# Optimization experiments

Hardware: AMD Instinct MI355X
Metric: run time of the kernel (lower is better)

## Reference

```python
import jax, jax.numpy as jnp
import numpy as np

N = 20480      # total nodes
E = 327680     # total edges (avg degree 16)
B = 16         # graphs in batch
IN = 16        # node feature dim
H = 8          # hidden_out_channel
CO = 64        # conv_out_channel
ET = 36        # n_edge_types
EF = 2         # edge_features
OUT = 1        # classifier out
DIMS = [(IN, H), (H, H), (H, H), (H, CO)]


def setup_inputs() -> dict:
    key = jax.random.key(0)
    ks = jax.random.split(key, 32)
    inp = {}
    inp['x'] = jax.random.normal(ks[0], (N, IN), jnp.float32)
    inp['edge_index'] = jax.random.randint(ks[1], (2, E), 0, N)
    inp['edge_type'] = jax.random.randint(ks[2], (E,), 0, ET)
    inp['edge_attr'] = jax.random.normal(ks[3], (E, EF), jnp.float32)
    inp['cell_type'] = jax.random.randint(ks[4], (N,), 0, 2)
    inp['batch'] = (jnp.arange(N) // (N // B)).astype(jnp.int32)
    i = 5
    for l, (ci, co) in enumerate(DIMS, 1):
        d = ci * co
        s = 1.0 / np.sqrt(EF)
        inp[f'emb{l}'] = jax.random.normal(ks[i], (ET, d), jnp.float32) * 0.02; i += 1
        inp[f'wh{l}'] = jax.random.normal(ks[i], (EF, d), jnp.float32) * s; i += 1
        inp[f'bh{l}'] = jnp.zeros((d,), jnp.float32)
        inp[f'wg{l}'] = jax.random.normal(ks[i], (EF, d), jnp.float32) * s; i += 1
        inp[f'bg{l}'] = jnp.zeros((d,), jnp.float32)
        inp[f'root{l}'] = jax.random.normal(ks[i], (ci, co), jnp.float32) / np.sqrt(ci); i += 1
        inp[f'bias{l}'] = jnp.zeros((co,), jnp.float32)
    inp['clf_w'] = jax.random.normal(ks[i], (CO, OUT), jnp.float32) / np.sqrt(CO)
    inp['clf_b'] = jnp.zeros((OUT,), jnp.float32)
    return inp


def edge_weights(etype, ef, emb, wh, bh, wg, bg):
    # EdgeNN: relu(embedding(type) * fc_h(feat) + fc_g(feat)) -> [E, cin*cout]
    return jax.nn.relu(emb[etype] * (ef @ wh + bh) + (ef @ wg + bg))


def nnconv(h, src, dst, W, root, bias):
    # NNConv(aggr='mean', root_weight=True): gather src feats, per-edge matmul, scatter-mean
    cin, cout = root.shape
    msg = jnp.einsum('ei,eio->eo', h[src], W.reshape(-1, cin, cout))  # [E, cout]
    agg = jax.ops.segment_sum(msg, dst, num_segments=N)
    deg = jax.ops.segment_sum(jnp.ones_like(msg[:, 0]), dst, num_segments=N)
    return agg / jnp.maximum(deg, 1.0)[:, None] + h @ root + bias


def reference(x, edge_index, edge_type, edge_attr, cell_type, batch,
              emb1, wh1, bh1, wg1, bg1, root1, bias1,
              emb2, wh2, bh2, wg2, bg2, root2, bias2,
              emb3, wh3, bh3, wg3, bg3, root3, bias3,
              emb4, wh4, bh4, wg4, bg4, root4, bias4,
              clf_w, clf_b):
    src, dst = edge_index[0], edge_index[1]
    layers = [(emb1, wh1, bh1, wg1, bg1, root1, bias1),
              (emb2, wh2, bh2, wg2, bg2, root2, bias2),
              (emb3, wh3, bh3, wg3, bg3, root3, bias3),
              (emb4, wh4, bh4, wg4, bg4, root4, bias4)]
    h = x
    for (emb, wh, bh, wg, bg, root, bias) in layers:  # fixed 4 structurally-distinct layers
        W = edge_weights(edge_type, edge_attr, emb, wh, bh, wg, bg)
        h = jax.nn.relu(nnconv(h, src, dst, W, root, bias))
    # gated scatter-mean pooling over tumor cells (cell_type == 1)
    gate = (cell_type == 1).astype(jnp.int32)
    seg = gate * (batch.astype(jnp.int32) + 1)  # 0 = masked-out bucket
    pooled = jax.ops.segment_sum(h, seg, num_segments=B + 1)
    cnt = jax.ops.segment_sum(jnp.ones((h.shape[0],), h.dtype), seg, num_segments=B + 1)
    pooled = (pooled / jnp.maximum(cnt, 1.0)[:, None])[1:B + 1]  # [B, CO]
    return jax.nn.sigmoid(pooled @ clf_w + clf_b)  # hazards [B, OUT]
```

## Files before the change

### kernel.cpp

```cpp
#include <hip/hip_runtime.h>
#include <math.h>

#define NN 20480
#define NE 327680
#define NBATCH 16

typedef float v2f __attribute__((ext_vector_type(2)));

static __device__ __forceinline__ v2f vmax0(v2f a) {
  v2f r; r.x = fmaxf(a.x, 0.f); r.y = fmaxf(a.y, 0.f); return r;
}
#define VMAX0 vmax0

__global__ __launch_bounds__(256) void prep_kernel(
    const int* __restrict__ dst, int* __restrict__ cnt,
    const float* __restrict__ e4, float* __restrict__ t4) {
  int b = blockIdx.x;
  if (b < NE / 256) {
    int e = b * 256 + threadIdx.x;
    atomicAdd(&cnt[dst[e]], 1);
  } else {
    int idx = (b - NE / 256) * 256 + threadIdx.x;
    int t = idx >> 9, r = idx & 511, o = r >> 3, i = r & 7;
    t4[idx] = e4[(t << 9) + i * 64 + o];
  }
}

__global__ __launch_bounds__(1024) void scan_kernel(const int* __restrict__ cnt,
                                                    int* __restrict__ off,
                                                    int* __restrict__ cur,
                                                    float* __restrict__ poolz) {
  __shared__ int part[1024];
  int tid = threadIdx.x;
  if (tid < NBATCH * 64 + NBATCH) poolz[tid] = 0.f;
  const int PT = NN / 1024;
  int loc[PT];
  int run = 0;
  int base = tid * PT;
#pragma unroll
  for (int k = 0; k < PT; k++) { loc[k] = run; run += cnt[base + k]; }
  part[tid] = run;
  __syncthreads();
  for (int d = 1; d < 1024; d <<= 1) {
    int t = (tid >= d) ? part[tid - d] : 0;
    __syncthreads();
    part[tid] += t;
    __syncthreads();
  }
  int pre = (tid == 0) ? 0 : part[tid - 1];
#pragma unroll
  for (int k = 0; k < PT; k++) {
    off[base + k] = pre + loc[k];
    cur[base + k] = pre + loc[k];
  }
  if (tid == 1023) off[NN] = pre + run;
}

__global__ void scatter_kernel(const int* __restrict__ src, const int* __restrict__ dst,
                               const int* __restrict__ etype, const float* __restrict__ eattr,
                               int* __restrict__ cur, float4* __restrict__ es) {
  int e = blockIdx.x * blockDim.x + threadIdx.x;
  if (e >= NE) return;
  int d = dst[e];
  int pos = atomicAdd(&cur[d], 1);
  es[pos] = make_float4(__int_as_float(src[e]), __int_as_float(etype[e]),
                        eattr[2 * e], eattr[2 * e + 1]);
}

__global__ __launch_bounds__(256) void layer_small16(
    const int* __restrict__ off, const float4* __restrict__ es,
    const float* __restrict__ h_in,
    const float* __restrict__ emb, const float* __restrict__ wh,
    const float* __restrict__ bh, const float* __restrict__ wg,
    const float* __restrict__ bg,
    const float* __restrict__ root, const float* __restrict__ bias,
    float* __restrict__ h_out) {
  constexpr int D = 128;
  constexpr int S = D + 1;
  __shared__ float semb[36 * S];
  for (int idx = threadIdx.x; idx < 36 * D; idx += 256) {
    int t = idx / D, io = idx - t * D;
    semb[t * S + io] = emb[idx];
  }
  int lane = threadIdx.x & 63;
  int o = lane & 7;
  int ihalf = (lane >> 3) & 1;
  int esub = lane >> 4;
  int ibase = ihalf * 8;
  v2f rwh0[4], rwh1[4], rbh[4], rwg0[4], rwg1[4], rbg[4], rroot[4];
#pragma unroll
  for (int p = 0; p < 4; p++) {
    int a = (ibase + 2 * p) * 8 + o, b = (ibase + 2 * p + 1) * 8 + o;
    rwh0[p] = (v2f){wh[a], wh[b]};
    rwh1[p] = (v2f){wh[D + a], wh[D + b]};
    rbh[p]  = (v2f){bh[a], bh[b]};
    rwg0[p] = (v2f){wg[a], wg[b]};
    rwg1[p] = (v2f){wg[D + a], wg[D + b]};
    rbg[p]  = (v2f){bg[a], bg[b]};
    rroot[p] = (v2f){root[a], root[b]};
  }
  float rbias = bias[o];
  __syncthreads();
  int wid = __builtin_amdgcn_readfirstlane(blockIdx.x * 4 + (threadIdx.x >> 6));
  for (int k = 0; k < 2; k++) {
    int n = wid * 2 + k;
    int beg = off[n], end = off[n + 1];
    float acc = 0.f;
    for (int j = beg + esub; j < end; j += 4) {
      float4 rec = es[j];
      int s = __float_as_int(rec.x);
      int t = __float_as_int(rec.y);
      v2f ef0 = (v2f){rec.z, rec.z}, ef1 = (v2f){rec.w, rec.w};
      const float4* hp = (const float4*)(h_in + s * 16 + ibase);
      float4 h0 = hp[0], h1 = hp[1];
      v2f hv[4] = {(v2f){h0.x, h0.y}, (v2f){h0.z, h0.w},
                   (v2f){h1.x, h1.y}, (v2f){h1.z, h1.w}};
      const float* st = &semb[t * S + ibase * 8 + o];
      v2f msg = {0.f, 0.f};
#pragma unroll
      for (int p = 0; p < 4; p++) {
        v2f hval = ef0 * rwh0[p] + ef1 * rwh1[p] + rbh[p];
        v2f gval = ef0 * rwg0[p] + ef1 * rwg1[p] + rbg[p];
        v2f stv = (v2f){st[(2 * p) * 8], st[(2 * p + 1) * 8]};
        msg += hv[p] * VMAX0(stv * hval + gval);
      }
      acc += msg.x + msg.y;
    }
    acc += __shfl_xor(acc, 8);
    acc += __shfl_xor(acc, 16);
    acc += __shfl_xor(acc, 32);
    const float* hn = h_in + n * 16 + ibase;
    v2f rtv = {0.f, 0.f};
#pragma unroll
    for (int p = 0; p < 4; p++)
      rtv += (v2f){hn[2 * p], hn[2 * p + 1]} * rroot[p];
    float rt = rtv.x + rtv.y;
    rt += __shfl_xor(rt, 8);
    float deg = (float)(end - beg);
    float val = fmaxf(rbias + rt + acc / fmaxf(deg, 1.f), 0.f);
    if (lane < 8) h_out[n * 8 + o] = val;
  }
}

__global__ __launch_bounds__(256) void layer_small8(
    const int* __restrict__ off, const float4* __restrict__ es,
    const float* __restrict__ h_in,
    const float* __restrict__ emb, const float* __restrict__ wh,
    const float* __restrict__ bh, const float* __restrict__ wg,
    const float* __restrict__ bg,
    const float* __restrict__ root, const float* __restrict__ bias,
    float* __restrict__ h_out) {
  constexpr int D = 64;
  constexpr int S = D + 1;
  __shared__ float semb[36 * S];
  for (int idx = threadIdx.x; idx < 36 * D; idx += 256) {
    int t = idx / D, io = idx - t * D;
    semb[t * S + io] = emb[idx];
  }
  int lane = threadIdx.x & 63;
  int o = lane & 7, esub = lane >> 3;
  v2f rwh0[4], rwh1[4], rbh[4], rwg0[4], rwg1[4], rbg[4], rroot[4];
#pragma unroll
  for (int p = 0; p < 4; p++) {
    int a = (2 * p) * 8 + o, b = (2 * p + 1) * 8 + o;
    rwh0[p] = (v2f){wh[a], wh[b]};
    rwh1[p] = (v2f){wh[D + a], wh[D + b]};
    rbh[p]  = (v2f){bh[a], bh[b]};
    rwg0[p] = (v2f){wg[a], wg[b]};
    rwg1[p] = (v2f){wg[D + a], wg[D + b]};
    rbg[p]  = (v2f){bg[a], bg[b]};
    rroot[p] = (v2f){root[a], root[b]};
  }
  float rbias = bias[o];
  __syncthreads();
  int wid = __builtin_amdgcn_readfirstlane(blockIdx.x * 4 + (threadIdx.x >> 6));
  for (int k = 0; k < 4; k++) {
    int n = wid * 4 + k;
    int beg = off[n], end = off[n + 1];
    float acc = 0.f;
    for (int j = beg + esub; j < end; j += 8) {
      float4 rec = es[j];
      int s = __float_as_int(rec.x);
      int t = __float_as_int(rec.y);
      v2f ef0 = (v2f){rec.z, rec.z}, ef1 = (v2f){rec.w, rec.w};
      const float4* hp = (const float4*)(h_in + s * 8);
      float4 h0 = hp[0], h1 = hp[1];
      v2f hv[4] = {(v2f){h0.x, h0.y}, (v2f){h0.z, h0.w},
                   (v2f){h1.x, h1.y}, (v2f){h1.z, h1.w}};
      const float* st = &semb[t * S + o];
      v2f msg = {0.f, 0.f};
#pragma unroll
      for (int p = 0; p < 4; p++) {
        v2f hval = ef0 * rwh0[p] + ef1 * rwh1[p] + rbh[p];
        v2f gval = ef0 * rwg0[p] + ef1 * rwg1[p] + rbg[p];
        v2f stv = (v2f){st[(2 * p) * 8], st[(2 * p + 1) * 8]};
        msg += hv[p] * VMAX0(stv * hval + gval);
      }
      acc += msg.x + msg.y;
    }
    acc += __shfl_xor(acc, 8);
    acc += __shfl_xor(acc, 16);
    acc += __shfl_xor(acc, 32);
    float deg = (float)(end - beg);
    const float* hn = h_in + n * 8;
    v2f rtv = {0.f, 0.f};
#pragma unroll
    for (int p = 0; p < 4; p++)
      rtv += (v2f){hn[2 * p], hn[2 * p + 1]} * rroot[p];
    float val = fmaxf(rbias + rtv.x + rtv.y + acc / fmaxf(deg, 1.f), 0.f);
    if (lane < 8) h_out[n * 8 + o] = val;
  }
}

__global__ __launch_bounds__(256) void layer_l4(
    const int* __restrict__ off, const float4* __restrict__ es,
    const float* __restrict__ h_in, const float* __restrict__ embT,
    const float* __restrict__ wh, const float* __restrict__ bh,
    const float* __restrict__ wg, const float* __restrict__ bg,
    const float* __restrict__ root, const float* __restrict__ bias,
    float* __restrict__ h_out) {
  int lane = threadIdx.x & 63;
  v2f rwh0[4], rwh1[4], rbh[4], rwg0[4], rwg1[4], rbg[4], rroot[4];
#pragma unroll
  for (int p = 0; p < 4; p++) {
    int a = (2 * p) * 64 + lane, b = (2 * p + 1) * 64 + lane;
    rwh0[p] = (v2f){wh[a], wh[b]};
    rwh1[p] = (v2f){wh[512 + a], wh[512 + b]};
    rbh[p]  = (v2f){bh[a], bh[b]};
    rwg0[p] = (v2f){wg[a], wg[b]};
    rwg1[p] = (v2f){wg[512 + a], wg[512 + b]};
    rbg[p]  = (v2f){bg[a], bg[b]};
    rroot[p] = (v2f){root[a], root[b]};
  }
  float rbias = bias[lane];
  int n = __builtin_amdgcn_readfirstlane((int)(blockIdx.x * 4) + (int)(threadIdx.x >> 6));
  int beg = off[n], end = off[n + 1];
  float acc0 = 0.f, acc1 = 0.f;
  int e = beg;
  for (; e + 2 <= end; e += 2) {
    float4 r0 = es[e], r1 = es[e + 1];
    int s0 = __float_as_int(r0.x), t0 = __float_as_int(r0.y);
    int s1 = __float_as_int(r1.x), t1 = __float_as_int(r1.y);
    const float4* hp0 = (const float4*)(h_in + s0 * 8);
    const float4* hp1 = (const float4*)(h_in + s1 * 8);
    float4 a0 = hp0[0], a1 = hp0[1];
    float4 b0 = hp1[0], b1 = hp1[1];
    const float4* ep0 = (const float4*)(embT + t0 * 512 + lane * 8);
    const float4* ep1 = (const float4*)(embT + t1 * 512 + lane * 8);
    float4 s00 = ep0[0], s01 = ep0[1];
    float4 s10 = ep1[0], s11 = ep1[1];
    v2f sv0[4] = {(v2f){s00.x, s00.y}, (v2f){s00.z, s00.w},
                  (v2f){s01.x, s01.y}, (v2f){s01.z, s01.w}};
    v2f sv1[4] = {(v2f){s10.x, s10.y}, (v2f){s10.z, s10.w},
                  (v2f){s11.x, s11.y}, (v2f){s11.z, s11.w}};
    v2f hva[4] = {(v2f){a0.x, a0.y}, (v2f){a0.z, a0.w},
                  (v2f){a1.x, a1.y}, (v2f){a1.z, a1.w}};
    v2f hvb[4] = {(v2f){b0.x, b0.y}, (v2f){b0.z, b0.w},
                  (v2f){b1.x, b1.y}, (v2f){b1.z, b1.w}};
    v2f e00 = (v2f){r0.z, r0.z}, e01 = (v2f){r0.w, r0.w};
    v2f e10 = (v2f){r1.z, r1.z}, e11 = (v2f){r1.w, r1.w};
    v2f m0 = {0.f, 0.f}, m1 = {0.f, 0.f};
#pragma unroll
    for (int p = 0; p < 4; p++) {
      v2f hv0 = e00 * rwh0[p] + e01 * rwh1[p] + rbh[p];
      v2f gv0 = e00 * rwg0[p] + e01 * rwg1[p] + rbg[p];
      m0 += hva[p] * VMAX0(sv0[p] * hv0 + gv0);
      v2f hv1 = e10 * rwh0[p] + e11 * rwh1[p] + rbh[p];
      v2f gv1 = e10 * rwg0[p] + e11 * rwg1[p] + rbg[p];
      m1 += hvb[p] * VMAX0(sv1[p] * hv1 + gv1);
    }
    acc0 += m0.x + m0.y;
    acc1 += m1.x + m1.y;
  }
  if (e < end) {
    float4 r0 = es[e];
    int s0 = __float_as_int(r0.x), t0 = __float_as_int(r0.y);
    const float4* hp0 = (const float4*)(h_in + s0 * 8);
    float4 a0 = hp0[0], a1 = hp0[1];
    const float4* ep0 = (const float4*)(embT + t0 * 512 + lane * 8);
    float4 s00 = ep0[0], s01 = ep0[1];
    v2f sv0[4] = {(v2f){s00.x, s00.y}, (v2f){s00.z, s00.w},
                  (v2f){s01.x, s01.y}, (v2f){s01.z, s01.w}};
    v2f hva[4] = {(v2f){a0.x, a0.y}, (v2f){a0.z, a0.w},
                  (v2f){a1.x, a1.y}, (v2f){a1.z, a1.w}};
    v2f e00 = (v2f){r0.z, r0.z}, e01 = (v2f){r0.w, r0.w};
    v2f m0 = {0.f, 0.f};
#pragma unroll
    for (int p = 0; p < 4; p++) {
      v2f hv0 = e00 * rwh0[p] + e01 * rwh1[p] + rbh[p];
      v2f gv0 = e00 * rwg0[p] + e01 * rwg1[p] + rbg[p];
      m0 += hva[p] * VMAX0(sv0[p] * hv0 + gv0);
    }
    acc0 += m0.x + m0.y;
  }
  float acc = acc0 + acc1;
  float deg = (float)(end - beg);
  const float* hn = h_in + n * 8;
  v2f rtv = {0.f, 0.f};
#pragma unroll
  for (int p = 0; p < 4; p++)
    rtv += (v2f){hn[2 * p], hn[2 * p + 1]} * rroot[p];
  h_out[n * 64 + lane] = fmaxf(rbias + rtv.x + rtv.y + acc / fmaxf(deg, 1.f), 0.f);
}

__global__ __launch_bounds__(256) void pool1_kernel(
    const float* __restrict__ h4, const int* __restrict__ ct,
    float* __restrict__ pooled, float* __restrict__ pcnt) {
  __shared__ float ss[4][64];
  __shared__ float sc[4];
  int b = blockIdx.x / 20, c = blockIdx.x % 20;
  int base = b * (NN / NBATCH) + c * 64;
  int o = threadIdx.x & 63, sub = threadIdx.x >> 6;
  float sum = 0.f, cnt = 0.f;
  for (int j = sub; j < 64; j += 4) {
    int n = base + j;
    if (ct[n] == 1) { sum += h4[n * 64 + o]; cnt += 1.f; }
  }
  ss[sub][o] = sum;
  if (o == 0) sc[sub] = cnt;
  __syncthreads();
  if (threadIdx.x < 64) {
    float tot = ss[0][o] + ss[1][o] + ss[2][o] + ss[3][o];
    unsafeAtomicAdd(&pooled[b * 64 + o], tot);
    if (o == 0) unsafeAtomicAdd(&pcnt[b], sc[0] + sc[1] + sc[2] + sc[3]);
  }
}

__global__ __launch_bounds__(1024) void pool2_kernel(
    const float* __restrict__ pooled, const float* __restrict__ pcnt,
    const float* __restrict__ clf_w, const float* __restrict__ clf_b,
    float* __restrict__ out) {
  int b = threadIdx.x >> 6, o = threadIdx.x & 63;
  float c = pcnt[b];
  float v = (pooled[b * 64 + o] / fmaxf(c, 1.f)) * clf_w[o];
#pragma unroll
  for (int d = 32; d; d >>= 1) v += __shfl_down(v, d);
  if (o == 0) out[b] = 1.f / (1.f + expf(-(v + clf_b[0])));
}

extern "C" void kernel_launch(void* const* d_in, const int* in_sizes, int n_in,
                              void* d_out, int out_size, void* d_ws, size_t ws_size,
                              hipStream_t stream) {
  (void)in_sizes; (void)n_in; (void)out_size; (void)ws_size;
  const float* x     = (const float*)d_in[0];
  const int*   eidx  = (const int*)d_in[1];
  const int*   src   = eidx;
  const int*   dst   = eidx + NE;
  const int*   etype = (const int*)d_in[2];
  const float* eattr = (const float*)d_in[3];
  const int*   ct    = (const int*)d_in[4];
  const float *emb[4], *wh[4], *bh[4], *wg[4], *bg[4], *root[4], *bias[4];
  for (int l = 0; l < 4; l++) {
    int b0 = 6 + 7 * l;
    emb[l]  = (const float*)d_in[b0 + 0];
    wh[l]   = (const float*)d_in[b0 + 1];
    bh[l]   = (const float*)d_in[b0 + 2];
    wg[l]   = (const float*)d_in[b0 + 3];
    bg[l]   = (const float*)d_in[b0 + 4];
    root[l] = (const float*)d_in[b0 + 5];
    bias[l] = (const float*)d_in[b0 + 6];
  }
  const float* clf_w = (const float*)d_in[34];
  const float* clf_b = (const float*)d_in[35];
  float* outp = (float*)d_out;

  float* ws  = (float*)d_ws;
  int*    off    = (int*)ws;
  float4* es     = (float4*)(ws + 20484);
  float*  hA     = ws + 20484 + 4 * NE;
  float*  hB     = hA + 8 * NN;
  float*  h4     = hB + 8 * NN;
  float*  embT4  = h4 + 64 * NN;
  float*  pooled = embT4 + 36 * 512;
  float*  pcnt   = pooled + 16 * 64;
  int*    cnt    = (int*)h4;
  int*    cur    = cnt + NN;

  hipMemsetAsync(cnt, 0, NN * sizeof(int), stream);
  prep_kernel<<<NE / 256 + 72, 256, 0, stream>>>(dst, cnt, emb[3], embT4);
  scan_kernel<<<1, 1024, 0, stream>>>(cnt, off, cur, pooled);
  scatter_kernel<<<NE / 256, 256, 0, stream>>>(src, dst, etype, eattr, cur, es);

  layer_small16<<<2560, 256, 0, stream>>>(off, es, x,
      emb[0], wh[0], bh[0], wg[0], bg[0], root[0], bias[0], hA);
  layer_small8<<<1280, 256, 0, stream>>>(off, es, hA,
      emb[1], wh[1], bh[1], wg[1], bg[1], root[1], bias[1], hB);
  layer_small8<<<1280, 256, 0, stream>>>(off, es, hB,
      emb[2], wh[2], bh[2], wg[2], bg[2], root[2], bias[2], hA);
  layer_l4<<<NN / 4, 256, 0, stream>>>(off, es, hA, embT4,
      wh[3], bh[3], wg[3], bg[3], root[3], bias[3], h4);

  pool1_kernel<<<320, 256, 0, stream>>>(h4, ct, pooled, pcnt);
  pool2_kernel<<<1, 1024, 0, stream>>>(pooled, pcnt, clf_w, clf_b, outp);
}
```

Baseline: 293.5 us.

## Fuse gated pooling into layer 4 and software-pipeline edge loads

Layer 4 now accumulates its output straight into the per-graph pooled sums with atomics, for tumor cells only. This removes the 64-wide h4 write, the separate pool1 kernel and its launch. The edge loop is restructured into a two-stage software pipeline that prefetches the next pair's source features and embedding rows while computing the current pair. In exchange there is more register pressure and many more float atomics on a small set of pooled addresses, which may contend.

```diff
diff --git a/kernel.cpp b/kernel.cpp
--- a/kernel.cpp
+++ b/kernel.cpp
@@ -212,15 +212,16 @@
   }
 }
 
-__global__ __launch_bounds__(256) void layer_l4(
+__global__ __launch_bounds__(256) void layer_l4p(
     const int* __restrict__ off, const float4* __restrict__ es,
     const float* __restrict__ h_in, const float* __restrict__ embT,
     const float* __restrict__ wh, const float* __restrict__ bh,
     const float* __restrict__ wg, const float* __restrict__ bg,
     const float* __restrict__ root, const float* __restrict__ bias,
-    float* __restrict__ h_out) {
+    const int* __restrict__ ct,
+    float* __restrict__ pooled, float* __restrict__ pcnt) {
   int lane = threadIdx.x & 63;
-  v2f rwh0[4], rwh1[4], rbh[4], rwg0[4], rwg1[4], rbg[4], rroot[4];
+  v2f rwh0[4], rwh1[4], rbh[4], rwg0[4], rwg1[4], rbg[4];
 #pragma unroll
   for (int p = 0; p < 4; p++) {
     int a = (2 * p) * 64 + lane, b = (2 * p + 1) * 64 + lane;
@@ -230,50 +231,73 @@
     rwg0[p] = (v2f){wg[a], wg[b]};
     rwg1[p] = (v2f){wg[512 + a], wg[512 + b]};
     rbg[p]  = (v2f){bg[a], bg[b]};
-    rroot[p] = (v2f){root[a], root[b]};
-  }
-  float rbias = bias[lane];
+  }
   int n = __builtin_amdgcn_readfirstlane((int)(blockIdx.x * 4) + (int)(threadIdx.x >> 6));
   int beg = off[n], end = off[n + 1];
+  int degi = end - beg;
+  int npair = degi >> 1;
   float acc0 = 0.f, acc1 = 0.f;
-  int e = beg;
-  for (; e + 2 <= end; e += 2) {
-    float4 r0 = es[e], r1 = es[e + 1];
-    int s0 = __float_as_int(r0.x), t0 = __float_as_int(r0.y);
-    int s1 = __float_as_int(r1.x), t1 = __float_as_int(r1.y);
+
+  float4 rA0, rA1, rB0, rB1;
+  float4 hA00, hA01, hA10, hA11, sA00, sA01, sA10, sA11;
+  if (npair > 0) { rA0 = es[beg]; rA1 = es[beg + 1]; }
+  if (npair > 1) { rB0 = es[beg + 2]; rB1 = es[beg + 3]; }
+  if (npair > 0) {
+    int s0 = __float_as_int(rA0.x), t0 = __float_as_int(rA0.y);
+    int s1 = __float_as_int(rA1.x), t1 = __float_as_int(rA1.y);
     const float4* hp0 = (const float4*)(h_in + s0 * 8);
     const float4* hp1 = (const float4*)(h_in + s1 * 8);
-    float4 a0 = hp0[0], a1 = hp0[1];
-    float4 b0 = hp1[0], b1 = hp1[1];
     const float4* ep0 = (const float4*)(embT + t0 * 512 + lane * 8);
     const float4* ep1 = (const float4*)(embT + t1 * 512 + lane * 8);
-    float4 s00 = ep0[0], s01 = ep0[1];
-    float4 s10 = ep1[0], s11 = ep1[1];
-    v2f sv0[4] = {(v2f){s00.x, s00.y}, (v2f){s00.z, s00.w},
-                  (v2f){s01.x, s01.y}, (v2f){s01.z, s01.w}};
-    v2f sv1[4] = {(v2f){s10.x, s10.y}, (v2f){s10.z, s10.w},
-                  (v2f){s11.x, s11.y}, (v2f){s11.z, s11.w}};
-    v2f hva[4] = {(v2f){a0.x, a0.y}, (v2f){a0.z, a0.w},
-                  (v2f){a1.x, a1.y}, (v2f){a1.z, a1.w}};
-    v2f hvb[4] = {(v2f){b0.x, b0.y}, (v2f){b0.z, b0.w},
-                  (v2f){b1.x, b1.y}, (v2f){b1.z, b1.w}};
-    v2f e00 = (v2f){r0.z, r0.z}, e01 = (v2f){r0.w, r0.w};
-    v2f e10 = (v2f){r1.z, r1.z}, e11 = (v2f){r1.w, r1.w};
-    v2f m0 = {0.f, 0.f}, m1 = {0.f, 0.f};
-#pragma unroll
-    for (int p = 0; p < 4; p++) {
-      v2f hv0 = e00 * rwh0[p] + e01 * rwh1[p] + rbh[p];
-      v2f gv0 = e00 * rwg0[p] + e01 * rwg1[p] + rbg[p];
-      m0 += hva[p] * VMAX0(sv0[p] * hv0 + gv0);
-      v2f hv1 = e10 * rwh0[p] + e11 * rwh1[p] + rbh[p];
-      v2f gv1 = e10 * rwg0[p] + e11 * rwg1[p] + rbg[p];
-      m1 += hvb[p] * VMAX0(sv1[p] * hv1 + gv1);
-    }
-    acc0 += m0.x + m0.y;
-    acc1 += m1.x + m1.y;
-  }
-  if (e < end) {
-    float4 r0 = es[e];
+    hA00 = hp0[0]; hA01 = hp0[1]; hA10 = hp1[0]; hA11 = hp1[1];
+    sA00 = ep0[0]; sA01 = ep0[1]; sA10 = ep1[0]; sA11 = ep1[1];
+  }
+#pragma unroll 2
+  for (int it = 0; it < npair; ++it) {
+    int eC = beg + 2 * it + 4;
+    int eCc = (eC + 1 < end) ? eC : beg;
+    float4 rC0 = es[eCc], rC1 = es[eCc + 1];
+    float4 hB00, hB01, hB10, hB11, sB00, sB01, sB10, sB11;
+    if (it + 1 < npair) {
+      int s0 = __float_as_int(rB0.x), t0 = __float_as_int(rB0.y);
+      int s1 = __float_as_int(rB1.x), t1 = __float_as_int(rB1.y);
+      const float4* hp0 = (const float4*)(h_in + s0 * 8);
+      const float4* hp1 = (const float4*)(h_in + s1 * 8);
+      const float4* ep0 = (const float4*)(embT + t0 * 512 + lane * 8);
+      const float4* ep1 = (const float4*)(embT + t1 * 512 + lane * 8);
+      hB00 = hp0[0]; hB01 = hp0[1]; hB10 = hp1[0]; hB11 = hp1[1];
+      sB00 = ep0[0]; sB01 = ep0[1]; sB10 = ep1[0]; sB11 = ep1[1];
+    }
+    {
+      v2f sv0[4] = {(v2f){sA00.x, sA00.y}, (v2f){sA00.z, sA00.w},
+                    (v2f){sA01.x, sA01.y}, (v2f){sA01.z, sA01.w}};
+      v2f sv1[4] = {(v2f){sA10.x, sA10.y}, (v2f){sA10.z, sA10.w},
+                    (v2f){sA11.x, sA11.y}, (v2f){sA11.z, sA11.w}};
+      v2f hva[4] = {(v2f){hA00.x, hA00.y}, (v2f){hA00.z, hA00.w},
+                    (v2f){hA01.x, hA01.y}, (v2f){hA01.z, hA01.w}};
+      v2f hvb[4] = {(v2f){hA10.x, hA10.y}, (v2f){hA10.z, hA10.w},
+                    (v2f){hA11.x, hA11.y}, (v2f){hA11.z, hA11.w}};
+      v2f e00 = (v2f){rA0.z, rA0.z}, e01 = (v2f){rA0.w, rA0.w};
+      v2f e10 = (v2f){rA1.z, rA1.z}, e11 = (v2f){rA1.w, rA1.w};
+      v2f m0 = {0.f, 0.f}, m1 = {0.f, 0.f};
+#pragma unroll
+      for (int p = 0; p < 4; p++) {
+        v2f hv0 = e00 * rwh0[p] + e01 * rwh1[p] + rbh[p];
+        v2f gv0 = e00 * rwg0[p] + e01 * rwg1[p] + rbg[p];
+        m0 += hva[p] * VMAX0(sv0[p] * hv0 + gv0);
+        v2f hv1 = e10 * rwh0[p] + e11 * rwh1[p] + rbh[p];
+        v2f gv1 = e10 * rwg0[p] + e11 * rwg1[p] + rbg[p];
+        m1 += hvb[p] * VMAX0(sv1[p] * hv1 + gv1);
+      }
+      acc0 += m0.x + m0.y;
+      acc1 += m1.x + m1.y;
+    }
+    rA0 = rB0; rA1 = rB1; rB0 = rC0; rB1 = rC1;
+    hA00 = hB00; hA01 = hB01; hA10 = hB10; hA11 = hB11;
+    sA00 = sB00; sA01 = sB01; sA10 = sB10; sA11 = sB11;
+  }
+  if (degi & 1) {
+    float4 r0 = es[end - 1];
     int s0 = __float_as_int(r0.x), t0 = __float_as_int(r0.y);
     const float4* hp0 = (const float4*)(h_in + s0 * 8);
     float4 a0 = hp0[0], a1 = hp0[1];
@@ -294,35 +318,16 @@
     acc0 += m0.x + m0.y;
   }
   float acc = acc0 + acc1;
-  float deg = (float)(end - beg);
+  float deg = (float)degi;
   const float* hn = h_in + n * 8;
-  v2f rtv = {0.f, 0.f};
-#pragma unroll
-  for (int p = 0; p < 4; p++)
-    rtv += (v2f){hn[2 * p], hn[2 * p + 1]} * rroot[p];
-  h_out[n * 64 + lane] = fmaxf(rbias + rtv.x + rtv.y + acc / fmaxf(deg, 1.f), 0.f);
-}
-
-__global__ __launch_bounds__(256) void pool1_kernel(
-    const float* __restrict__ h4, const int* __restrict__ ct,
-    float* __restrict__ pooled, float* __restrict__ pcnt) {
-  __shared__ float ss[4][64];
-  __shared__ float sc[4];
-  int b = blockIdx.x / 20, c = blockIdx.x % 20;
-  int base = b * (NN / NBATCH) + c * 64;
-  int o = threadIdx.x & 63, sub = threadIdx.x >> 6;
-  float sum = 0.f, cnt = 0.f;
-  for (int j = sub; j < 64; j += 4) {
-    int n = base + j;
-    if (ct[n] == 1) { sum += h4[n * 64 + o]; cnt += 1.f; }
-  }
-  ss[sub][o] = sum;
-  if (o == 0) sc[sub] = cnt;
-  __syncthreads();
-  if (threadIdx.x < 64) {
-    float tot = ss[0][o] + ss[1][o] + ss[2][o] + ss[3][o];
-    unsafeAtomicAdd(&pooled[b * 64 + o], tot);
-    if (o == 0) unsafeAtomicAdd(&pcnt[b], sc[0] + sc[1] + sc[2] + sc[3]);
+  float rt = bias[lane];
+#pragma unroll
+  for (int i = 0; i < 8; i++) rt = fmaf(hn[i], root[i * 64 + lane], rt);
+  float val = fmaxf(rt + acc / fmaxf(deg, 1.f), 0.f);
+  if (ct[n] == 1) {
+    int b = n / (NN / NBATCH);
+    unsafeAtomicAdd(&pooled[b * 64 + lane], val);
+    if (lane == 0) unsafeAtomicAdd(&pcnt[b], 1.0f);
   }
 }
 
@@ -387,9 +392,8 @@
       emb[1], wh[1], bh[1], wg[1], bg[1], root[1], bias[1], hB);
   layer_small8<<<1280, 256, 0, stream>>>(off, es, hB,
       emb[2], wh[2], bh[2], wg[2], bg[2], root[2], bias[2], hA);
-  layer_l4<<<NN / 4, 256, 0, stream>>>(off, es, hA, embT4,
-      wh[3], bh[3], wg[3], bg[3], root[3], bias[3], h4);
-
-  pool1_kernel<<<320, 256, 0, stream>>>(h4, ct, pooled, pcnt);
+  layer_l4p<<<NN / 4, 256, 0, stream>>>(off, es, hA, embT4,
+      wh[3], bh[3], wg[3], bg[3], root[3], bias[3], ct, pooled, pcnt);
+
   pool2_kernel<<<1, 1024, 0, stream>>>(pooled, pcnt, clf_w, clf_b, outp);
 }
```

After: 394.6 us. +34.4%, slower.

## Fuse layer-4 with gated pooling and split edges across two waves per node

Applied to the files above, without the earlier changes.

The final conv layer now writes no h4 buffer. Each node's result is atomically added straight into the per-graph pooled sums, which removes the separate pool1 pass and the 64-wide node-feature write and read. Layer 4 also splits each node's edge list between two wavefronts and combines their partial sums through shared memory, doubling the number of blocks. The smaller layers drop their per-wave node loops (one node per wave for layer 1, two for layers 2-3) to expose more parallelism. The cost is many more float atomics on the 16x64 pooled array, plus a block-level sync in layer 4.

```diff
diff --git a/kernel.cpp b/kernel.cpp
--- a/kernel.cpp
+++ b/kernel.cpp
@@ -29,10 +29,12 @@
 __global__ __launch_bounds__(1024) void scan_kernel(const int* __restrict__ cnt,
                                                     int* __restrict__ off,
                                                     int* __restrict__ cur,
-                                                    float* __restrict__ poolz) {
+                                                    float* __restrict__ pooled,
+                                                    float* __restrict__ pcnt) {
   __shared__ int part[1024];
   int tid = threadIdx.x;
-  if (tid < NBATCH * 64 + NBATCH) poolz[tid] = 0.f;
+  pooled[tid] = 0.f;
+  if (tid < NBATCH) pcnt[tid] = 0.f;
   const int PT = NN / 1024;
   int loc[PT];
   int run = 0;
@@ -101,45 +103,42 @@
   }
   float rbias = bias[o];
   __syncthreads();
-  int wid = __builtin_amdgcn_readfirstlane(blockIdx.x * 4 + (threadIdx.x >> 6));
-  for (int k = 0; k < 2; k++) {
-    int n = wid * 2 + k;
-    int beg = off[n], end = off[n + 1];
-    float acc = 0.f;
-    for (int j = beg + esub; j < end; j += 4) {
-      float4 rec = es[j];
-      int s = __float_as_int(rec.x);
-      int t = __float_as_int(rec.y);
-      v2f ef0 = (v2f){rec.z, rec.z}, ef1 = (v2f){rec.w, rec.w};
-      const float4* hp = (const float4*)(h_in + s * 16 + ibase);
-      float4 h0 = hp[0], h1 = hp[1];
-      v2f hv[4] = {(v2f){h0.x, h0.y}, (v2f){h0.z, h0.w},
-                   (v2f){h1.x, h1.y}, (v2f){h1.z, h1.w}};
-      const float* st = &semb[t * S + ibase * 8 + o];
-      v2f msg = {0.f, 0.f};
-#pragma unroll
-      for (int p = 0; p < 4; p++) {
-        v2f hval = ef0 * rwh0[p] + ef1 * rwh1[p] + rbh[p];
-        v2f gval = ef0 * rwg0[p] + ef1 * rwg1[p] + rbg[p];
-        v2f stv = (v2f){st[(2 * p) * 8], st[(2 * p + 1) * 8]};
-        msg += hv[p] * VMAX0(stv * hval + gval);
-      }
-      acc += msg.x + msg.y;
-    }
-    acc += __shfl_xor(acc, 8);
-    acc += __shfl_xor(acc, 16);
-    acc += __shfl_xor(acc, 32);
-    const float* hn = h_in + n * 16 + ibase;
-    v2f rtv = {0.f, 0.f};
-#pragma unroll
-    for (int p = 0; p < 4; p++)
-      rtv += (v2f){hn[2 * p], hn[2 * p + 1]} * rroot[p];
-    float rt = rtv.x + rtv.y;
-    rt += __shfl_xor(rt, 8);
-    float deg = (float)(end - beg);
-    float val = fmaxf(rbias + rt + acc / fmaxf(deg, 1.f), 0.f);
-    if (lane < 8) h_out[n * 8 + o] = val;
-  }
+  int n = __builtin_amdgcn_readfirstlane(blockIdx.x * 4 + (threadIdx.x >> 6));
+  int beg = off[n], end = off[n + 1];
+  float acc = 0.f;
+  for (int j = beg + esub; j < end; j += 4) {
+    float4 rec = es[j];
+    int s = __float_as_int(rec.x);
+    int t = __float_as_int(rec.y);
+    v2f ef0 = (v2f){rec.z, rec.z}, ef1 = (v2f){rec.w, rec.w};
+    const float4* hp = (const float4*)(h_in + s * 16 + ibase);
+    float4 h0 = hp[0], h1 = hp[1];
+    v2f hv[4] = {(v2f){h0.x, h0.y}, (v2f){h0.z, h0.w},
+                 (v2f){h1.x, h1.y}, (v2f){h1.z, h1.w}};
+    const float* st = &semb[t * S + ibase * 8 + o];
+    v2f msg = {0.f, 0.f};
+#pragma unroll
+    for (int p = 0; p < 4; p++) {
+      v2f hval = ef0 * rwh0[p] + ef1 * rwh1[p] + rbh[p];
+      v2f gval = ef0 * rwg0[p] + ef1 * rwg1[p] + rbg[p];
+      v2f stv = (v2f){st[(2 * p) * 8], st[(2 * p + 1) * 8]};
+      msg += hv[p] * VMAX0(stv * hval + gval);
+    }
+    acc += msg.x + msg.y;
+  }
+  acc += __shfl_xor(acc, 8);
+  acc += __shfl_xor(acc, 16);
+  acc += __shfl_xor(acc, 32);
+  const float* hn = h_in + n * 16 + ibase;
+  v2f rtv = {0.f, 0.f};
+#pragma unroll
+  for (int p = 0; p < 4; p++)
+    rtv += (v2f){hn[2 * p], hn[2 * p + 1]} * rroot[p];
+  float rt = rtv.x + rtv.y;
+  rt += __shfl_xor(rt, 8);
+  float deg = (float)(end - beg);
+  float val = fmaxf(rbias + rt + acc / fmaxf(deg, 1.f), 0.f);
+  if (lane < 8) h_out[n * 8 + o] = val;
 }
 
 __global__ __launch_bounds__(256) void layer_small8(
@@ -174,8 +173,8 @@
   float rbias = bias[o];
   __syncthreads();
   int wid = __builtin_amdgcn_readfirstlane(blockIdx.x * 4 + (threadIdx.x >> 6));
-  for (int k = 0; k < 4; k++) {
-    int n = wid * 4 + k;
+  for (int k = 0; k < 2; k++) {
+    int n = wid * 2 + k;
     int beg = off[n], end = off[n + 1];
     float acc = 0.f;
     for (int j = beg + esub; j < end; j += 8) {
@@ -212,14 +211,19 @@
   }
 }
 
-__global__ __launch_bounds__(256) void layer_l4(
+__global__ __launch_bounds__(256) void layer_l4x(
     const int* __restrict__ off, const float4* __restrict__ es,
     const float* __restrict__ h_in, const float* __restrict__ embT,
     const float* __restrict__ wh, const float* __restrict__ bh,
     const float* __restrict__ wg, const float* __restrict__ bg,
     const float* __restrict__ root, const float* __restrict__ bias,
-    float* __restrict__ h_out) {
-  int lane = threadIdx.x & 63;
+    const int* __restrict__ ct,
+    float* __restrict__ pooled, float* __restrict__ pcnt) {
+  __shared__ float comb[2][64];
+  int tid = threadIdx.x;
+  int lane = tid & 63;
+  int wid = tid >> 6;
+  int nodeSub = wid >> 1, half = wid & 1;
   v2f rwh0[4], rwh1[4], rbh[4], rwg0[4], rwg1[4], rbg[4], rroot[4];
 #pragma unroll
   for (int p = 0; p < 4; p++) {
@@ -233,11 +237,15 @@
     rroot[p] = (v2f){root[a], root[b]};
   }
   float rbias = bias[lane];
-  int n = __builtin_amdgcn_readfirstlane((int)(blockIdx.x * 4) + (int)(threadIdx.x >> 6));
+  int n = __builtin_amdgcn_readfirstlane((int)(blockIdx.x * 2) + nodeSub);
   int beg = off[n], end = off[n + 1];
+  int len = end - beg;
+  int len0 = (len + 1) >> 1;
+  int wbeg = half ? (beg + len0) : beg;
+  int wend = half ? end : (beg + len0);
   float acc0 = 0.f, acc1 = 0.f;
-  int e = beg;
-  for (; e + 2 <= end; e += 2) {
+  int e = wbeg;
+  for (; e + 2 <= wend; e += 2) {
     float4 r0 = es[e], r1 = es[e + 1];
     int s0 = __float_as_int(r0.x), t0 = __float_as_int(r0.y);
     int s1 = __float_as_int(r1.x), t1 = __float_as_int(r1.y);
@@ -272,7 +280,7 @@
     acc0 += m0.x + m0.y;
     acc1 += m1.x + m1.y;
   }
-  if (e < end) {
+  if (e < wend) {
     float4 r0 = es[e];
     int s0 = __float_as_int(r0.x), t0 = __float_as_int(r0.y);
     const float4* hp0 = (const float4*)(h_in + s0 * 8);
@@ -294,35 +302,22 @@
     acc0 += m0.x + m0.y;
   }
   float acc = acc0 + acc1;
-  float deg = (float)(end - beg);
-  const float* hn = h_in + n * 8;
-  v2f rtv = {0.f, 0.f};
-#pragma unroll
-  for (int p = 0; p < 4; p++)
-    rtv += (v2f){hn[2 * p], hn[2 * p + 1]} * rroot[p];
-  h_out[n * 64 + lane] = fmaxf(rbias + rtv.x + rtv.y + acc / fmaxf(deg, 1.f), 0.f);
-}
-
-__global__ __launch_bounds__(256) void pool1_kernel(
-    const float* __restrict__ h4, const int* __restrict__ ct,
-    float* __restrict__ pooled, float* __restrict__ pcnt) {
-  __shared__ float ss[4][64];
-  __shared__ float sc[4];
-  int b = blockIdx.x / 20, c = blockIdx.x % 20;
-  int base = b * (NN / NBATCH) + c * 64;
-  int o = threadIdx.x & 63, sub = threadIdx.x >> 6;
-  float sum = 0.f, cnt = 0.f;
-  for (int j = sub; j < 64; j += 4) {
-    int n = base + j;
-    if (ct[n] == 1) { sum += h4[n * 64 + o]; cnt += 1.f; }
-  }
-  ss[sub][o] = sum;
-  if (o == 0) sc[sub] = cnt;
+  if (half) comb[nodeSub][lane] = acc;
   __syncthreads();
-  if (threadIdx.x < 64) {
-    float tot = ss[0][o] + ss[1][o] + ss[2][o] + ss[3][o];
-    unsafeAtomicAdd(&pooled[b * 64 + o], tot);
-    if (o == 0) unsafeAtomicAdd(&pcnt[b], sc[0] + sc[1] + sc[2] + sc[3]);
+  if (!half) {
+    acc += comb[nodeSub][lane];
+    float deg = (float)len;
+    const float* hn = h_in + n * 8;
+    v2f rtv = {0.f, 0.f};
+#pragma unroll
+    for (int p = 0; p < 4; p++)
+      rtv += (v2f){hn[2 * p], hn[2 * p + 1]} * rroot[p];
+    float val = fmaxf(rbias + rtv.x + rtv.y + acc / fmaxf(deg, 1.f), 0.f);
+    if (ct[n] == 1) {
+      int b = n / (NN / NBATCH);
+      unsafeAtomicAdd(&pooled[b * 64 + lane], val);
+      if (lane == 0) unsafeAtomicAdd(&pcnt[b], 1.0f);
+    }
   }
 }
 
@@ -369,27 +364,26 @@
   float4* es     = (float4*)(ws + 20484);
   float*  hA     = ws + 20484 + 4 * NE;
   float*  hB     = hA + 8 * NN;
-  float*  h4     = hB + 8 * NN;
-  float*  embT4  = h4 + 64 * NN;
+  float*  scratch= hB + 8 * NN;
+  float*  embT4  = scratch + 64 * NN;
   float*  pooled = embT4 + 36 * 512;
   float*  pcnt   = pooled + 16 * 64;
-  int*    cnt    = (int*)h4;
+  int*    cnt    = (int*)scratch;
   int*    cur    = cnt + NN;
 
   hipMemsetAsync(cnt, 0, NN * sizeof(int), stream);
   prep_kernel<<<NE / 256 + 72, 256, 0, stream>>>(dst, cnt, emb[3], embT4);
-  scan_kernel<<<1, 1024, 0, stream>>>(cnt, off, cur, pooled);
+  scan_kernel<<<1, 1024, 0, stream>>>(cnt, off, cur, pooled, pcnt);
   scatter_kernel<<<NE / 256, 256, 0, stream>>>(src, dst, etype, eattr, cur, es);
 
-  layer_small16<<<2560, 256, 0, stream>>>(off, es, x,
+  layer_small16<<<NN / 4, 256, 0, stream>>>(off, es, x,
       emb[0], wh[0], bh[0], wg[0], bg[0], root[0], bias[0], hA);
-  layer_small8<<<1280, 256, 0, stream>>>(off, es, hA,
+  layer_small8<<<NN / 8, 256, 0, stream>>>(off, es, hA,
       emb[1], wh[1], bh[1], wg[1], bg[1], root[1], bias[1], hB);
-  layer_small8<<<1280, 256, 0, stream>>>(off, es, hB,
+  layer_small8<<<NN / 8, 256, 0, stream>>>(off, es, hB,
       emb[2], wh[2], bh[2], wg[2], bg[2], root[2], bias[2], hA);
-  layer_l4<<<NN / 4, 256, 0, stream>>>(off, es, hA, embT4,
-      wh[3], bh[3], wg[3], bg[3], root[3], bias[3], h4);
-
-  pool1_kernel<<<320, 256, 0, stream>>>(h4, ct, pooled, pcnt);
+  layer_l4x<<<NN / 2, 256, 0, stream>>>(off, es, hA, embT4,
+      wh[3], bh[3], wg[3], bg[3], root[3], bias[3], ct, pooled, pcnt);
+
   pool2_kernel<<<1, 1024, 0, stream>>>(pooled, pcnt, clf_w, clf_b, outp);
 }
```

New measurement: 405.1 us. 1.38x slower.
